# Kernel optimization log

Measured on AMD Instinct MI355X. Metric: run time of the kernel, lower is better.

The kernel has to match this reference:

```python
import jax, jax.numpy as jnp
import numpy as np

N, E, M = 20000, 320000, 64
LOG2 = float(np.log(2.0))
INV_SQRT_M = 1.0 / float(np.sqrt(M))
PW_S = float(np.sqrt(1.0 / 5.0))   # path weight for 0e-output paths: sqrt(ir_out.dim / n_paths)
PW_V = float(np.sqrt(3.0 / 5.0))   # path weight for 1e-output paths
INV_SQRT3 = 1.0 / float(np.sqrt(3.0))
INV_SQRT2 = 1.0 / float(np.sqrt(2.0))


def ssp(x):  # ShiftedSoftPlus
    return jax.nn.softplus(x) - LOG2


def split(feat):
    return feat[:, :M], feat[:, M:].reshape(feat.shape[0], M, 3)


def e3_linear(feat, W0, b0, W1):
    # e3nn o3.Linear per irrep group, fan-in normalized; bias only on scalar (0e) irreps
    s, v = split(feat)
    s = s @ (W0 * INV_SQRT_M) + b0
    v = jnp.einsum('nui,uv->nvi', v, W1 * INV_SQRT_M)
    return jnp.concatenate([s, v.reshape(v.shape[0], 3 * M)], axis=-1)


def fcnet(h, Ws):
    # e3nn FullyConnectedNet: no biases, fan-in normalized, ssp between layers
    for i, W in enumerate(Ws):
        h = h @ (W * (1.0 / float(np.sqrt(W.shape[0]))))
        if i < len(Ws) - 1:
            h = ssp(h)
    return h


def setup_inputs() -> dict:
    key = jax.random.key(0)
    ks = jax.random.split(key, 24)
    r = lambda i, shape: jax.random.normal(ks[i], shape, dtype=jnp.float32)
    inp = {
        'x': r(0, (N, 4 * M)),
        'edge_index': jax.random.randint(ks[1], (2, E), 0, N, dtype=jnp.int64)
        if jax.config.jax_enable_x64 else jax.random.randint(ks[1], (2, E), 0, N),
        'edge_sh': r(2, (E, 4)),
        'edge_attr': r(3, (E, 64)),
        # linear_node_pre
        'W_pre0': r(4, (M, M)), 'b_pre0': jnp.zeros((M,), jnp.float32), 'W_pre1': r(5, (M, M)),
        # NormGate fc (plain torch nn.Linear with bias)
        'Wg1': r(6, (2 * M, 2 * M)) * 0.08, 'bg1': jnp.zeros((2 * M,), jnp.float32),
        'Wg2': r(7, (2 * M, 2 * M)) * 0.08, 'bg2': jnp.zeros((2 * M,), jnp.float32),
        # linear_node
        'Wn0': r(8, (M, M)), 'bn0': jnp.zeros((M,), jnp.float32), 'Wn1': r(9, (M, M)),
        # fc_node: [edge_attr_dim=64, 32, weight_numel=5*M]
        'Wf1': r(10, (64, 32)), 'Wf2': r(11, (32, 5 * M)),
        # layer_l0: [192, 32, 5*M]
        'Wl1': r(12, (192, 32)), 'Wl2': r(13, (32, 5 * M)),
        # linear_out
        'Wo0': r(14, (M, M)), 'bo0': jnp.zeros((M,), jnp.float32), 'Wo1': r(15, (M, M)),
    }
    return inp


def reference(x, edge_index, edge_sh, edge_attr,
              W_pre0, b_pre0, W_pre1, Wg1, bg1, Wg2, bg2,
              Wn0, bn0, Wn1, Wf1, Wf2, Wl1, Wl2, Wo0, bo0, Wo1):
    edge_dst, edge_src = edge_index[0], edge_index[1]

    # --- pre linear + edge invariants s0 ---
    pre_x = e3_linear(x, W_pre0, b_pre0, W_pre1)
    ps, pv = split(pre_x)
    # InnerProduct on 1e group (uuu, path weight 1/ir.dim): mean over m of elementwise product
    ip1 = jnp.einsum('eui,eui->eu', pv[edge_dst], pv[edge_src]) * (1.0 / 3.0)  # [E, M]
    s0 = jnp.concatenate([ps[edge_dst], ps[edge_dst], ip1], axis=-1)  # [E, 192]

    # --- NormGate ---
    xs, xv = split(x)
    norm_v = jnp.sqrt(jnp.sum(xv * xv, axis=-1) + 1e-12)  # [N, M]
    f0 = jnp.concatenate([xs, norm_v], axis=-1)  # [N, 2M]
    g = jax.nn.silu(f0 @ Wg1 + bg1) @ Wg2 + bg2  # [N, 2M]
    gated = xv * g[:, M:, None]
    xg = jnp.concatenate([g[:, :M], gated.reshape(N, 3 * M)], axis=-1)

    xg = e3_linear(xg, Wn0, bn0, Wn1)
    self_x = xg

    # --- per-edge tensor product weights ---
    w = (fcnet(edge_attr, [Wf1, Wf2]) * fcnet(s0, [Wl1, Wl2])).reshape(E, 5, M)

    # --- edge-wise equivariant tensor product (uvu, 5 paths) ---
    gs, gv = split(xg)
    es, ev = gs[edge_src], gv[edge_src]            # [E,M], [E,M,3]
    sh0, sh1 = edge_sh[:, 0], edge_sh[:, 1:4]      # [E], [E,3]

    out_s = PW_S * (w[:, 0] * es * sh0[:, None]
                    + w[:, 3] * jnp.einsum('eui,ei->eu', ev, sh1) * INV_SQRT3)
    cross = jnp.cross(ev, sh1[:, None, :])
    out_v = PW_V * (w[:, 1][:, :, None] * es[:, :, None] * sh1[:, None, :]
                    + w[:, 2][:, :, None] * ev * sh0[:, None, None]
                    + w[:, 4][:, :, None] * cross * INV_SQRT2)
    edge_feat = jnp.concatenate([out_s, out_v.reshape(E, 3 * M)], axis=-1)  # [E, 4M]

    # --- scatter aggregate to destination nodes ---
    out = jax.ops.segment_sum(edge_feat, edge_dst, num_segments=N)
    out = out + self_x  # irrep_in_node == irrep_out
    out = e3_linear(out, Wo0, bo0, Wo1)
    return out
```

## Files before the change

kernel.cpp:

```cpp
#include <hip/hip_runtime.h>
#include <math.h>

#define NNODE 20000
#define NEDGE 320000

__device__ __forceinline__ float sspf(float x) {
    return fmaxf(x, 0.f) + log1pf(expf(-fabsf(x))) - 0.6931471805599453f;
}

__global__ __launch_bounds__(256) void k_e3lin(
    const float* __restrict__ in, const float* __restrict__ add,
    float* __restrict__ out,
    const float* __restrict__ W0, const float* __restrict__ b0,
    const float* __restrict__ W1, int nrows)
{
    __shared__ float sW0[64 * 64];
    __shared__ float sW1[64 * 64];
    __shared__ float sb0[64];
    __shared__ float srow[4][256];
    const int tid = threadIdx.x;
    for (int i = tid; i < 64 * 16; i += 256) {
        ((float4*)sW0)[i] = ((const float4*)W0)[i];
        ((float4*)sW1)[i] = ((const float4*)W1)[i];
    }
    if (tid < 64) sb0[tid] = b0[tid];
    __syncthreads();

    const int rr = tid >> 6;
    const int v  = tid & 63;
    for (int r0 = blockIdx.x * 4; r0 < nrows; r0 += gridDim.x * 4) {
        {
            int i = tid;
            int r = i >> 6, c = i & 63;
            int row = r0 + r;
            float4 val = make_float4(0.f, 0.f, 0.f, 0.f);
            if (row < nrows) {
                val = ((const float4*)(in + (size_t)row * 256))[c];
                if (add) {
                    float4 a = ((const float4*)(add + (size_t)row * 256))[c];
                    val.x += a.x; val.y += a.y; val.z += a.z; val.w += a.w;
                }
            }
            ((float4*)srow[r])[c] = val;
        }
        __syncthreads();

        int row = r0 + rr;
        if (row < nrows) {
            const float* rw = srow[rr];
            float s = 0.f, a0 = 0.f, a1 = 0.f, a2 = 0.f;
            #pragma unroll 16
            for (int u = 0; u < 64; ++u) {
                float w0 = sW0[u * 64 + v];
                float w1 = sW1[u * 64 + v];
                s  += rw[u] * w0;
                a0 += rw[64 + u * 3 + 0] * w1;
                a1 += rw[64 + u * 3 + 1] * w1;
                a2 += rw[64 + u * 3 + 2] * w1;
            }
            out[row * 256 + v]              = s  * 0.125f + sb0[v];
            out[row * 256 + 64 + v * 3 + 0] = a0 * 0.125f;
            out[row * 256 + 64 + v * 3 + 1] = a1 * 0.125f;
            out[row * 256 + 64 + v * 3 + 2] = a2 * 0.125f;
        }
        __syncthreads();
    }
}

__global__ __launch_bounds__(256) void k_gate(
    const float* __restrict__ x, float* __restrict__ xg,
    const float* __restrict__ Wg1, const float* __restrict__ bg1,
    const float* __restrict__ Wg2, const float* __restrict__ bg2,
    int nrows)
{
    __shared__ float sW1[128 * 128];
    __shared__ float sW2[128 * 128];
    __shared__ float sb1[128], sb2[128];
    __shared__ float srow[2][256];
    __shared__ float sf0[2][128];
    __shared__ float sh1[2][128];
    const int tid = threadIdx.x;
    for (int i = tid; i < 128 * 32; i += 256) {
        ((float4*)sW1)[i] = ((const float4*)Wg1)[i];
        ((float4*)sW2)[i] = ((const float4*)Wg2)[i];
    }
    if (tid < 128) { sb1[tid] = bg1[tid]; sb2[tid] = bg2[tid]; }
    __syncthreads();

    const int rr = tid >> 7;
    const int j  = tid & 127;
    for (int base = blockIdx.x * 2; base < nrows; base += gridDim.x * 2) {
        if (tid < 128) {
            int r = tid >> 6, c = tid & 63;
            int row = base + r;
            float4 v = make_float4(0.f, 0.f, 0.f, 0.f);
            if (row < nrows) v = ((const float4*)(x + (size_t)row * 256))[c];
            ((float4*)srow[r])[c] = v;
        }
        __syncthreads();
        {
            float f;
            if (j < 64) f = srow[rr][j];
            else {
                int u = j - 64;
                float v0 = srow[rr][64 + u * 3 + 0];
                float v1 = srow[rr][64 + u * 3 + 1];
                float v2 = srow[rr][64 + u * 3 + 2];
                f = sqrtf(v0 * v0 + v1 * v1 + v2 * v2 + 1e-12f);
            }
            sf0[rr][j] = f;
        }
        __syncthreads();
        {
            float acc = sb1[j];
            #pragma unroll 16
            for (int k = 0; k < 128; ++k) acc += sf0[rr][k] * sW1[k * 128 + j];
            sh1[rr][j] = acc / (1.f + expf(-acc));
        }
        __syncthreads();
        {
            float acc = sb2[j];
            #pragma unroll 16
            for (int k = 0; k < 128; ++k) acc += sh1[rr][k] * sW2[k * 128 + j];
            int row = base + rr;
            if (row < nrows) {
                if (j < 64) xg[row * 256 + j] = acc;
                else {
                    int u = j - 64;
                    xg[row * 256 + 64 + u * 3 + 0] = srow[rr][64 + u * 3 + 0] * acc;
                    xg[row * 256 + 64 + u * 3 + 1] = srow[rr][64 + u * 3 + 1] * acc;
                    xg[row * 256 + 64 + u * 3 + 2] = srow[rr][64 + u * 3 + 2] * acc;
                }
            }
        }
        __syncthreads();
    }
}

#define EPW 2
__global__ __launch_bounds__(1024, 4) void k_edge(
    const float* __restrict__ pre, const float* __restrict__ slf,
    const int* __restrict__ ei, const float* __restrict__ eshp,
    const float* __restrict__ ea,
    const float* __restrict__ Wf1, const float* __restrict__ Wf2,
    const float* __restrict__ Wl1, const float* __restrict__ Wl2,
    float* __restrict__ acc)
{
    __shared__ float2 sW1mb[64 * 64];
    __shared__ float4 sW2a[32 * 64];
    __shared__ float4 sW2b[32 * 64];
    __shared__ float2 sW2c[32 * 64];
    __shared__ float  sIN[16][EPW][192];
    __shared__ float  sH [16][EPW][64];
    const int tid = threadIdx.x;
    const float sc_f1 = 0.125f;
    const float sc_l1 = 0.07216878364870323f;
    const float sc_2  = 0.17677669529663687f;
    for (int i = tid; i < 64 * 64; i += 1024) {
        int u = i >> 6, c = i & 63, j = c & 31;
        float wm, wb;
        if (c < 32) {
            wm = Wf1[u * 32 + j] * sc_f1;
            wb = 0.f;
        } else {
            wm = (Wl1[u * 32 + j] + Wl1[(64 + u) * 32 + j]) * sc_l1;
            wb = Wl1[(128 + u) * 32 + j] * sc_l1;
        }
        sW1mb[i] = make_float2(wm, wb);
    }
    for (int i = tid; i < 32 * 64; i += 1024) {
        int jj = i >> 6, col = i & 63;
        const float* f2 = Wf2 + jj * 320 + col;
        const float* l2 = Wl2 + jj * 320 + col;
        sW2a[i] = make_float4(f2[0] * sc_2, f2[64] * sc_2, f2[128] * sc_2, f2[192] * sc_2);
        sW2b[i] = make_float4(l2[0] * sc_2, l2[64] * sc_2, l2[128] * sc_2, l2[192] * sc_2);
        sW2c[i] = make_float2(f2[256] * sc_2, l2[256] * sc_2);
    }
    __syncthreads();

    const int lane  = tid & 63;
    const int w     = tid >> 6;
    const int gwave = blockIdx.x * (blockDim.x >> 6) + w;
    const int nwav  = gridDim.x * (blockDim.x >> 6);
    const float* inb = &sIN[w][0][(lane >> 5) << 6];

    for (int base0 = gwave * EPW; base0 < NEDGE; base0 += nwav * EPW) {
        const int base = __builtin_amdgcn_readfirstlane(base0);
        int dstv[EPW], srcv[EPW];
        #pragma unroll
        for (int t = 0; t < EPW; ++t) {
            int e = base + t;
            int d = ei[e], s = ei[NEDGE + e];
            dstv[t] = d; srcv[t] = s;
            float psd = pre[d * 256 + lane];
            float pd0 = pre[d * 256 + 64 + lane * 3 + 0];
            float pd1 = pre[d * 256 + 64 + lane * 3 + 1];
            float pd2 = pre[d * 256 + 64 + lane * 3 + 2];
            float ps0 = pre[s * 256 + 64 + lane * 3 + 0];
            float ps1 = pre[s * 256 + 64 + lane * 3 + 1];
            float ps2 = pre[s * 256 + 64 + lane * 3 + 2];
            float ip1 = (pd0 * ps0 + pd1 * ps1 + pd2 * ps2) * (1.f / 3.f);
            float eav = ea[e * 64 + lane];
            sIN[w][t][lane]       = eav;
            sIN[w][t][64 + lane]  = psd;
            sIN[w][t][128 + lane] = ip1;
        }

        float hacc[EPW] = {0.f, 0.f};
        #pragma unroll 16
        for (int uu = 0; uu < 64; ++uu) {
            float2 wmb = sW1mb[uu * 64 + lane];
            #pragma unroll
            for (int t = 0; t < EPW; ++t) {
                float b1 = inb[t * 192 + uu];
                float bI = sIN[w][t][128 + uu];
                hacc[t] += b1 * wmb.x + bI * wmb.y;
            }
        }
        #pragma unroll
        for (int t = 0; t < EPW; ++t) sH[w][t][lane] = sspf(hacc[t]);

        float aA[EPW][5], aB[EPW][5];
        #pragma unroll
        for (int t = 0; t < EPW; ++t)
            #pragma unroll
            for (int k = 0; k < 5; ++k) { aA[t][k] = 0.f; aB[t][k] = 0.f; }
        #pragma unroll 8
        for (int jj = 0; jj < 32; ++jj) {
            float4 wa = sW2a[jj * 64 + lane];
            float4 wb = sW2b[jj * 64 + lane];
            float2 wc = sW2c[jj * 64 + lane];
            #pragma unroll
            for (int t = 0; t < EPW; ++t) {
                float hA = sH[w][t][jj];
                float hB = sH[w][t][32 + jj];
                aA[t][0] += hA * wa.x; aA[t][1] += hA * wa.y;
                aA[t][2] += hA * wa.z; aA[t][3] += hA * wa.w;
                aA[t][4] += hA * wc.x;
                aB[t][0] += hB * wb.x; aB[t][1] += hB * wb.y;
                aB[t][2] += hB * wb.z; aB[t][3] += hB * wb.w;
                aB[t][4] += hB * wc.y;
            }
        }

        #pragma unroll
        for (int t = 0; t < EPW; ++t) {
            int e = base + t;
            float w0 = aA[t][0] * aB[t][0];
            float w1 = aA[t][1] * aB[t][1];
            float w2 = aA[t][2] * aB[t][2];
            float w3 = aA[t][3] * aB[t][3];
            float w4 = aA[t][4] * aB[t][4];
            int s = srcv[t];
            float es  = slf[s * 256 + lane];
            float ev0 = slf[s * 256 + 64 + lane * 3 + 0];
            float ev1 = slf[s * 256 + 64 + lane * 3 + 1];
            float ev2 = slf[s * 256 + 64 + lane * 3 + 2];
            float s0v = eshp[e * 4 + 0];
            float sx  = eshp[e * 4 + 1];
            float sy  = eshp[e * 4 + 2];
            float sz  = eshp[e * 4 + 3];
            float dotv = ev0 * sx + ev1 * sy + ev2 * sz;
            const float PW_S = 0.4472135954999579f;
            const float PW_V = 0.7745966692414834f;
            const float IS3  = 0.5773502691896258f;
            const float IS2  = 0.7071067811865476f;
            float outs = PW_S * (w0 * es * s0v + w3 * dotv * IS3);
            float cx = ev1 * sz - ev2 * sy;
            float cy = ev2 * sx - ev0 * sz;
            float cz = ev0 * sy - ev1 * sx;
            float ov0 = PW_V * (w1 * es * sx + w2 * ev0 * s0v + w4 * cx * IS2);
            float ov1 = PW_V * (w1 * es * sy + w2 * ev1 * s0v + w4 * cy * IS2);
            float ov2 = PW_V * (w1 * es * sz + w2 * ev2 * s0v + w4 * cz * IS2);
            int d = dstv[t];
            atomicAdd(&acc[d * 256 + lane], outs);
            atomicAdd(&acc[d * 256 + 64 + lane * 3 + 0], ov0);
            atomicAdd(&acc[d * 256 + 64 + lane * 3 + 1], ov1);
            atomicAdd(&acc[d * 256 + 64 + lane * 3 + 2], ov2);
        }
    }
}

extern "C" void kernel_launch(void* const* d_in, const int* in_sizes, int n_in,
                              void* d_out, int out_size, void* d_ws, size_t ws_size,
                              hipStream_t stream) {
    const float* x     = (const float*)d_in[0];
    const int*   ei    = (const int*)  d_in[1];
    const float* esh   = (const float*)d_in[2];
    const float* eattr = (const float*)d_in[3];
    const float* Wpre0 = (const float*)d_in[4];
    const float* bpre0 = (const float*)d_in[5];
    const float* Wpre1 = (const float*)d_in[6];
    const float* Wg1   = (const float*)d_in[7];
    const float* bg1   = (const float*)d_in[8];
    const float* Wg2   = (const float*)d_in[9];
    const float* bg2   = (const float*)d_in[10];
    const float* Wn0   = (const float*)d_in[11];
    const float* bn0   = (const float*)d_in[12];
    const float* Wn1   = (const float*)d_in[13];
    const float* Wf1   = (const float*)d_in[14];
    const float* Wf2   = (const float*)d_in[15];
    const float* Wl1   = (const float*)d_in[16];
    const float* Wl2   = (const float*)d_in[17];
    const float* Wo0   = (const float*)d_in[18];
    const float* bo0   = (const float*)d_in[19];
    const float* Wo1   = (const float*)d_in[20];
    float* out = (float*)d_out;
    float* ws  = (float*)d_ws;

    float* pre = ws;
    float* xg  = ws + (size_t)NNODE * 256;
    float* slf = ws + (size_t)NNODE * 256 * 2;
    float* acc = ws + (size_t)NNODE * 256 * 3;

    hipMemsetAsync(acc, 0, (size_t)NNODE * 256 * sizeof(float), stream);
    k_e3lin<<<1280, 256, 0, stream>>>(x,  nullptr, pre, Wpre0, bpre0, Wpre1, NNODE);
    k_gate <<<512,  256, 0, stream>>>(x,  xg, Wg1, bg1, Wg2, bg2, NNODE);
    k_e3lin<<<1280, 256, 0, stream>>>(xg, nullptr, slf, Wn0, bn0, Wn1, NNODE);
    k_edge <<<256, 1024, 0, stream>>>(pre, slf, ei, esh, eattr, Wf1, Wf2, Wl1, Wl2, acc);
    k_e3lin<<<1280, 256, 0, stream>>>(acc, slf, out, Wo0, bo0, Wo1, NNODE);
}
```

Baseline: 1.204 ms.

## Sort edges by destination and accumulate per node instead of atomics

Each call now builds a CSR grouping of edges by destination node using a histogram, a single-block scan and an atomic scatter of edge indices. The edge kernel assigns one wave per destination node, loads the destination features once and accumulates all incoming edge contributions in registers. It then writes each output row once, which removes the per-edge float atomics and the accumulator memset. In exchange it adds three small preprocessing kernels per call, reads edge attributes in a gathered order, and wastes some compute on padded edge pairs when a node has an odd edge count.

Result: faster. 1.136 ms (-5.6%).

```diff
diff --git a/kernel.cpp b/kernel.cpp
--- a/kernel.cpp
+++ b/kernel.cpp
@@ -137,11 +137,58 @@
     }
 }
 
+__global__ __launch_bounds__(256) void k_hist(const int* __restrict__ ei, int* __restrict__ hist) {
+    int e = blockIdx.x * 256 + threadIdx.x;
+    if (e < NEDGE) atomicAdd(&hist[ei[e]], 1);
+}
+
+__global__ __launch_bounds__(1024) void k_scan(const int* __restrict__ hist,
+                                               int* __restrict__ offs,
+                                               int* __restrict__ curs) {
+    __shared__ int part[1024];
+    const int t = threadIdx.x;
+    const int base = t * 20;
+    int loc[20];
+    int s = 0;
+    #pragma unroll
+    for (int k = 0; k < 20; ++k) {
+        int b = base + k;
+        int v = (b < NNODE) ? hist[b] : 0;
+        loc[k] = s; s += v;
+    }
+    part[t] = s;
+    __syncthreads();
+    for (int off = 1; off < 1024; off <<= 1) {
+        int v = (t >= off) ? part[t - off] : 0;
+        __syncthreads();
+        part[t] += v;
+        __syncthreads();
+    }
+    int excl = (t == 0) ? 0 : part[t - 1];
+    #pragma unroll
+    for (int k = 0; k < 20; ++k) {
+        int b = base + k;
+        if (b < NNODE) { offs[b] = excl + loc[k]; curs[b] = excl + loc[k]; }
+    }
+    if (t == 1023) offs[NNODE] = part[1023];
+}
+
+__global__ __launch_bounds__(256) void k_scatteridx(const int* __restrict__ ei,
+                                                    int* __restrict__ curs,
+                                                    int* __restrict__ order) {
+    int e = blockIdx.x * 256 + threadIdx.x;
+    if (e < NEDGE) {
+        int p = atomicAdd(&curs[ei[e]], 1);
+        order[p] = e;
+    }
+}
+
 #define EPW 2
 __global__ __launch_bounds__(1024, 4) void k_edge(
     const float* __restrict__ pre, const float* __restrict__ slf,
     const int* __restrict__ ei, const float* __restrict__ eshp,
     const float* __restrict__ ea,
+    const int* __restrict__ offs, const int* __restrict__ order,
     const float* __restrict__ Wf1, const float* __restrict__ Wf2,
     const float* __restrict__ Wl1, const float* __restrict__ Wl2,
     float* __restrict__ acc)
@@ -184,100 +231,110 @@
     const int nwav  = gridDim.x * (blockDim.x >> 6);
     const float* inb = &sIN[w][0][(lane >> 5) << 6];
 
-    for (int base0 = gwave * EPW; base0 < NEDGE; base0 += nwav * EPW) {
-        const int base = __builtin_amdgcn_readfirstlane(base0);
-        int dstv[EPW], srcv[EPW];
-        #pragma unroll
-        for (int t = 0; t < EPW; ++t) {
-            int e = base + t;
-            int d = ei[e], s = ei[NEDGE + e];
-            dstv[t] = d; srcv[t] = s;
-            float psd = pre[d * 256 + lane];
-            float pd0 = pre[d * 256 + 64 + lane * 3 + 0];
-            float pd1 = pre[d * 256 + 64 + lane * 3 + 1];
-            float pd2 = pre[d * 256 + 64 + lane * 3 + 2];
-            float ps0 = pre[s * 256 + 64 + lane * 3 + 0];
-            float ps1 = pre[s * 256 + 64 + lane * 3 + 1];
-            float ps2 = pre[s * 256 + 64 + lane * 3 + 2];
-            float ip1 = (pd0 * ps0 + pd1 * ps1 + pd2 * ps2) * (1.f / 3.f);
-            float eav = ea[e * 64 + lane];
-            sIN[w][t][lane]       = eav;
-            sIN[w][t][64 + lane]  = psd;
-            sIN[w][t][128 + lane] = ip1;
-        }
-
-        float hacc[EPW] = {0.f, 0.f};
-        #pragma unroll 16
-        for (int uu = 0; uu < 64; ++uu) {
-            float2 wmb = sW1mb[uu * 64 + lane];
+    const float PW_S = 0.4472135954999579f;
+    const float PW_V = 0.7745966692414834f;
+    const float IS3  = 0.5773502691896258f;
+    const float IS2  = 0.7071067811865476f;
+
+    for (int d = gwave; d < NNODE; d += nwav) {
+        const int e0 = __builtin_amdgcn_readfirstlane(offs[d]);
+        const int e1 = __builtin_amdgcn_readfirstlane(offs[d + 1]);
+        float psd = pre[d * 256 + lane];
+        float pd0 = pre[d * 256 + 64 + lane * 3 + 0];
+        float pd1 = pre[d * 256 + 64 + lane * 3 + 1];
+        float pd2 = pre[d * 256 + 64 + lane * 3 + 2];
+        sIN[w][0][64 + lane] = psd;
+        sIN[w][1][64 + lane] = psd;
+
+        float accS = 0.f, aV0 = 0.f, aV1 = 0.f, aV2 = 0.f;
+
+        for (int i = e0; i < e1; i += EPW) {
+            const int cnt = e1 - i;
+            int eo[EPW], srcv[EPW];
             #pragma unroll
             for (int t = 0; t < EPW; ++t) {
-                float b1 = inb[t * 192 + uu];
-                float bI = sIN[w][t][128 + uu];
-                hacc[t] += b1 * wmb.x + bI * wmb.y;
-            }
-        }
-        #pragma unroll
-        for (int t = 0; t < EPW; ++t) sH[w][t][lane] = sspf(hacc[t]);
-
-        float aA[EPW][5], aB[EPW][5];
-        #pragma unroll
-        for (int t = 0; t < EPW; ++t)
+                int idx = (t < cnt) ? (i + t) : i;
+                int e = __builtin_amdgcn_readfirstlane(order[idx]);
+                int s = __builtin_amdgcn_readfirstlane(ei[NEDGE + e]);
+                eo[t] = e; srcv[t] = s;
+                float ps0 = pre[s * 256 + 64 + lane * 3 + 0];
+                float ps1 = pre[s * 256 + 64 + lane * 3 + 1];
+                float ps2 = pre[s * 256 + 64 + lane * 3 + 2];
+                float ip1 = (pd0 * ps0 + pd1 * ps1 + pd2 * ps2) * (1.f / 3.f);
+                float eav = ea[e * 64 + lane];
+                sIN[w][t][lane]       = eav;
+                sIN[w][t][128 + lane] = ip1;
+            }
+
+            float hacc[EPW] = {0.f, 0.f};
+            #pragma unroll 16
+            for (int uu = 0; uu < 64; ++uu) {
+                float2 wmb = sW1mb[uu * 64 + lane];
+                #pragma unroll
+                for (int t = 0; t < EPW; ++t) {
+                    float b1 = inb[t * 192 + uu];
+                    float bI = sIN[w][t][128 + uu];
+                    hacc[t] += b1 * wmb.x + bI * wmb.y;
+                }
+            }
             #pragma unroll
-            for (int k = 0; k < 5; ++k) { aA[t][k] = 0.f; aB[t][k] = 0.f; }
-        #pragma unroll 8
-        for (int jj = 0; jj < 32; ++jj) {
-            float4 wa = sW2a[jj * 64 + lane];
-            float4 wb = sW2b[jj * 64 + lane];
-            float2 wc = sW2c[jj * 64 + lane];
+            for (int t = 0; t < EPW; ++t) sH[w][t][lane] = sspf(hacc[t]);
+
+            float aA[EPW][5], aB[EPW][5];
+            #pragma unroll
+            for (int t = 0; t < EPW; ++t)
+                #pragma unroll
+                for (int k = 0; k < 5; ++k) { aA[t][k] = 0.f; aB[t][k] = 0.f; }
+            #pragma unroll 8
+            for (int jj = 0; jj < 32; ++jj) {
+                float4 wa = sW2a[jj * 64 + lane];
+                float4 wb = sW2b[jj * 64 + lane];
+                float2 wc = sW2c[jj * 64 + lane];
+                #pragma unroll
+                for (int t = 0; t < EPW; ++t) {
+                    float hA = sH[w][t][jj];
+                    float hB = sH[w][t][32 + jj];
+                    aA[t][0] += hA * wa.x; aA[t][1] += hA * wa.y;
+                    aA[t][2] += hA * wa.z; aA[t][3] += hA * wa.w;
+                    aA[t][4] += hA * wc.x;
+                    aB[t][0] += hB * wb.x; aB[t][1] += hB * wb.y;
+                    aB[t][2] += hB * wb.z; aB[t][3] += hB * wb.w;
+                    aB[t][4] += hB * wc.y;
+                }
+            }
+
             #pragma unroll
             for (int t = 0; t < EPW; ++t) {
-                float hA = sH[w][t][jj];
-                float hB = sH[w][t][32 + jj];
-                aA[t][0] += hA * wa.x; aA[t][1] += hA * wa.y;
-                aA[t][2] += hA * wa.z; aA[t][3] += hA * wa.w;
-                aA[t][4] += hA * wc.x;
-                aB[t][0] += hB * wb.x; aB[t][1] += hB * wb.y;
-                aB[t][2] += hB * wb.z; aB[t][3] += hB * wb.w;
-                aB[t][4] += hB * wc.y;
-            }
-        }
-
-        #pragma unroll
-        for (int t = 0; t < EPW; ++t) {
-            int e = base + t;
-            float w0 = aA[t][0] * aB[t][0];
-            float w1 = aA[t][1] * aB[t][1];
-            float w2 = aA[t][2] * aB[t][2];
-            float w3 = aA[t][3] * aB[t][3];
-            float w4 = aA[t][4] * aB[t][4];
-            int s = srcv[t];
-            float es  = slf[s * 256 + lane];
-            float ev0 = slf[s * 256 + 64 + lane * 3 + 0];
-            float ev1 = slf[s * 256 + 64 + lane * 3 + 1];
-            float ev2 = slf[s * 256 + 64 + lane * 3 + 2];
-            float s0v = eshp[e * 4 + 0];
-            float sx  = eshp[e * 4 + 1];
-            float sy  = eshp[e * 4 + 2];
-            float sz  = eshp[e * 4 + 3];
-            float dotv = ev0 * sx + ev1 * sy + ev2 * sz;
-            const float PW_S = 0.4472135954999579f;
-            const float PW_V = 0.7745966692414834f;
-            const float IS3  = 0.5773502691896258f;
-            const float IS2  = 0.7071067811865476f;
-            float outs = PW_S * (w0 * es * s0v + w3 * dotv * IS3);
-            float cx = ev1 * sz - ev2 * sy;
-            float cy = ev2 * sx - ev0 * sz;
-            float cz = ev0 * sy - ev1 * sx;
-            float ov0 = PW_V * (w1 * es * sx + w2 * ev0 * s0v + w4 * cx * IS2);
-            float ov1 = PW_V * (w1 * es * sy + w2 * ev1 * s0v + w4 * cy * IS2);
-            float ov2 = PW_V * (w1 * es * sz + w2 * ev2 * s0v + w4 * cz * IS2);
-            int d = dstv[t];
-            atomicAdd(&acc[d * 256 + lane], outs);
-            atomicAdd(&acc[d * 256 + 64 + lane * 3 + 0], ov0);
-            atomicAdd(&acc[d * 256 + 64 + lane * 3 + 1], ov1);
-            atomicAdd(&acc[d * 256 + 64 + lane * 3 + 2], ov2);
-        }
+                if (t >= cnt) break;
+                int e = eo[t], s = srcv[t];
+                float w0 = aA[t][0] * aB[t][0];
+                float w1 = aA[t][1] * aB[t][1];
+                float w2 = aA[t][2] * aB[t][2];
+                float w3 = aA[t][3] * aB[t][3];
+                float w4 = aA[t][4] * aB[t][4];
+                float es  = slf[s * 256 + lane];
+                float ev0 = slf[s * 256 + 64 + lane * 3 + 0];
+                float ev1 = slf[s * 256 + 64 + lane * 3 + 1];
+                float ev2 = slf[s * 256 + 64 + lane * 3 + 2];
+                float s0v = eshp[e * 4 + 0];
+                float sx  = eshp[e * 4 + 1];
+                float sy  = eshp[e * 4 + 2];
+                float sz  = eshp[e * 4 + 3];
+                float dotv = ev0 * sx + ev1 * sy + ev2 * sz;
+                accS += PW_S * (w0 * es * s0v + w3 * dotv * IS3);
+                float cx = ev1 * sz - ev2 * sy;
+                float cy = ev2 * sx - ev0 * sz;
+                float cz = ev0 * sy - ev1 * sx;
+                aV0 += PW_V * (w1 * es * sx + w2 * ev0 * s0v + w4 * cx * IS2);
+                aV1 += PW_V * (w1 * es * sy + w2 * ev1 * s0v + w4 * cy * IS2);
+                aV2 += PW_V * (w1 * es * sz + w2 * ev2 * s0v + w4 * cz * IS2);
+            }
+        }
+
+        acc[d * 256 + lane]              = accS;
+        acc[d * 256 + 64 + lane * 3 + 0] = aV0;
+        acc[d * 256 + 64 + lane * 3 + 1] = aV1;
+        acc[d * 256 + 64 + lane * 3 + 2] = aV2;
     }
 }
 
@@ -312,11 +369,20 @@
     float* xg  = ws + (size_t)NNODE * 256;
     float* slf = ws + (size_t)NNODE * 256 * 2;
     float* acc = ws + (size_t)NNODE * 256 * 3;
-
-    hipMemsetAsync(acc, 0, (size_t)NNODE * 256 * sizeof(float), stream);
+    int*   hist  = (int*)(ws + (size_t)NNODE * 256 * 4);
+    int*   offs  = hist + NNODE;
+    int*   curs  = offs + NNODE + 2;
+    int*   order = curs + NNODE;
+
+    hipMemsetAsync(hist, 0, NNODE * sizeof(int), stream);
+    k_hist      <<<(NEDGE + 255) / 256, 256, 0, stream>>>(ei, hist);
+    k_scan      <<<1, 1024, 0, stream>>>(hist, offs, curs);
+    k_scatteridx<<<(NEDGE + 255) / 256, 256, 0, stream>>>(ei, curs, order);
+
     k_e3lin<<<1280, 256, 0, stream>>>(x,  nullptr, pre, Wpre0, bpre0, Wpre1, NNODE);
     k_gate <<<512,  256, 0, stream>>>(x,  xg, Wg1, bg1, Wg2, bg2, NNODE);
     k_e3lin<<<1280, 256, 0, stream>>>(xg, nullptr, slf, Wn0, bn0, Wn1, NNODE);
-    k_edge <<<256, 1024, 0, stream>>>(pre, slf, ei, esh, eattr, Wf1, Wf2, Wl1, Wl2, acc);
+    k_edge <<<256, 1024, 0, stream>>>(pre, slf, ei, esh, eattr, offs, order,
+                                      Wf1, Wf2, Wl1, Wl2, acc);
     k_e3lin<<<1280, 256, 0, stream>>>(acc, slf, out, Wo0, bo0, Wo1, NNODE);
 }
```
